# Performance work log

Measured on AMD Instinct MI355X. Metric: run time of the kernel, lower is better.

The kernel has to match this reference:

```python
import jax, jax.numpy as jnp
import numpy as np

WS = 11  # window_size
PAD = WS // 2
C1 = 0.01 ** 2
C2 = 0.03 ** 2
_DN = ('NCHW', 'OIHW', 'NCHW')


def _box_filter(x):
    """Depthwise 11x11 uniform (1/121) box filter with zero padding,
    implemented as two separable 1D depthwise convs (math-identical to
    F.conv2d with the ones/ws^2 window and padding=ws//2)."""
    c = x.shape[1]
    kh = jnp.ones((c, 1, WS, 1), x.dtype) / WS
    kw = jnp.ones((c, 1, 1, WS), x.dtype) / WS
    x = jax.lax.conv_general_dilated(x, kh, (1, 1), [(PAD, PAD), (0, 0)],
                                     feature_group_count=c, dimension_numbers=_DN)
    x = jax.lax.conv_general_dilated(x, kw, (1, 1), [(0, 0), (PAD, PAD)],
                                     feature_group_count=c, dimension_numbers=_DN)
    return x


def setup_inputs() -> dict:
    key = jax.random.key(0)
    k1, k2 = jax.random.split(key)
    shape = (16, 3, 512, 512)
    img1 = jax.random.uniform(k1, shape, dtype=jnp.float32)
    img2 = jax.random.uniform(k2, shape, dtype=jnp.float32)
    return {"img1": img1, "img2": img2}


def reference(img1, img2):
    mu1 = _box_filter(img1)
    mu2 = _box_filter(img2)
    mu1_sq = mu1 * mu1
    mu2_sq = mu2 * mu2
    mu1_mu2 = mu1 * mu2
    sigma1_sq = _box_filter(img1 * img1) - mu1_sq
    sigma2_sq = _box_filter(img2 * img2) - mu2_sq
    sigma12 = _box_filter(img1 * img2) - mu1_mu2
    ssim_map = ((2.0 * mu1_mu2 + C1) * (2.0 * sigma12 + C2)) / (
        (mu1_sq + mu2_sq + C1) * (sigma1_sq + sigma2_sq + C2))
    return 1.0 - jnp.mean(ssim_map)
```

## Files before the change

### kernel.cpp

```cpp
#include <hip/hip_runtime.h>
#include <hip/hip_fp16.h>


#define CAP   28
#define ROWF  132
#define SSTR  (3 * ROWF)
#define C1K   1.4641f
#define C2K   13.1769f

__device__ __forceinline__ int swz(int x) { return x + (x >> 5); }

__launch_bounds__(256, 3)
__global__ void ssim_fused(const float* __restrict__ img1,
                           const float* __restrict__ img2,
                           float* __restrict__ out)
{
    __shared__ unsigned int ring[CAP * SSTR];

    const int x0 = blockIdx.x * 128;
    const int y0 = blockIdx.y * 128;
    const size_t pbase = (size_t)blockIdx.z * (512 * 512);
    const int tid = threadIdx.x;

    const int hj = tid >> 4;
    const int hk = tid & 15;
    const int xl = x0 + hk * 8 - 8;
    const int xs = swz(tid & 127);

    float S0 = 0.f, S1 = 0.f, S2 = 0.f, S3 = 0.f, S4 = 0.f, accs = 0.f;
    int pslot = hj;
    int cbase = 0;

    for (int t = 0; t < 19; ++t) {
        if (tid < 128) {
            if (t < 18) {
                const int rel = 8 * t + hj;
                const int r   = y0 - 5 + rel;
                float a[24], b[24];
                if ((unsigned)r < 512u) {
                    const float* p1 = img1 + pbase + (size_t)r * 512;
                    const float* p2 = img2 + pbase + (size_t)r * 512;
#pragma unroll
                    for (int u = 0; u < 6; ++u) {
                        const int c4 = xl + 4 * u;
                        float4 v1 = {0.f, 0.f, 0.f, 0.f};
                        float4 v2 = {0.f, 0.f, 0.f, 0.f};
                        if ((unsigned)c4 < 512u) {
                            v1 = *(const float4*)(p1 + c4);
                            v2 = *(const float4*)(p2 + c4);
                        }
                        a[4*u] = v1.x; a[4*u+1] = v1.y; a[4*u+2] = v1.z; a[4*u+3] = v1.w;
                        b[4*u] = v2.x; b[4*u+1] = v2.y; b[4*u+2] = v2.z; b[4*u+3] = v2.w;
                    }
                } else {
#pragma unroll
                    for (int u = 0; u < 24; ++u) { a[u] = 0.f; b[u] = 0.f; }
                }

                float w0 = 0.f, w1 = 0.f, w2 = 0.f, w3 = 0.f, w4 = 0.f;
#pragma unroll
                for (int c = 0; c < 11; ++c) {
                    const float av = a[c + 3], bv = b[c + 3];
                    w0 += av; w1 += bv; w2 += av * av; w3 += bv * bv; w4 += av * bv;
                }

                unsigned int* rb = &ring[pslot * SSTR];
#pragma unroll
                for (int i = 0; i < 8; ++i) {
                    const int ad = swz(hk * 8 + i);
                    const __half2 h01 = __floats2half2_rn(w0, w1);
                    const __half2 h23 = __floats2half2_rn(w2, w3);
                    const __half2 h4x = __floats2half2_rn(w4, 0.f);
                    rb[ad]            = *(const unsigned int*)&h01;
                    rb[ad + ROWF]     = *(const unsigned int*)&h23;
                    rb[ad + 2 * ROWF] = *(const unsigned int*)&h4x;
                    if (i < 7) {
                        const float aN = a[14 + i], aO = a[3 + i];
                        const float bN = b[14 + i], bO = b[3 + i];
                        w0 += aN - aO;
                        w1 += bN - bO;
                        w2 += aN * aN - aO * aO;
                        w3 += bN * bN - bO * bO;
                        w4 += aN * bN - aO * bO;
                    }
                }
                pslot += 8; if (pslot >= CAP) pslot -= CAP;
            }
        } else {
            if (t >= 1) {
#pragma unroll
                for (int jj = 0; jj < 8; ++jj) {
                    const int rel = 8 * (t - 1) + jj;
                    int sa = cbase + jj; if (sa >= CAP) sa -= CAP;
                    const unsigned int* ab = &ring[sa * SSTR + xs];
                    const unsigned int u01 = ab[0], u23 = ab[ROWF], u4 = ab[2 * ROWF];
                    const float2 f01 = __half22float2(*(const __half2*)&u01);
                    const float2 f23 = __half22float2(*(const __half2*)&u23);
                    const float2 f4v = __half22float2(*(const __half2*)&u4);
                    S0 += f01.x; S1 += f01.y; S2 += f23.x; S3 += f23.y; S4 += f4v.x;
                    if (rel >= 11) {
                        int ss = sa - 11; if (ss < 0) ss += CAP;
                        const unsigned int* sb = &ring[ss * SSTR + xs];
                        const unsigned int v01 = sb[0], v23 = sb[ROWF], v4 = sb[2 * ROWF];
                        const float2 g01 = __half22float2(*(const __half2*)&v01);
                        const float2 g23 = __half22float2(*(const __half2*)&v23);
                        const float2 g4v = __half22float2(*(const __half2*)&v4);
                        S0 -= g01.x; S1 -= g01.y; S2 -= g23.x; S3 -= g23.y; S4 -= g4v.x;
                    }
                    if (rel >= 10 && rel <= 137) {
                        const float t01 = S0 * S1;
                        const float p0  = S0 * S0, p1 = S1 * S1;
                        const float num = (2.f * t01 + C1K)
                                        * (2.f * (121.f * S4 - t01) + C2K);
                        const float den = (p0 + p1 + C1K)
                                        * (121.f * (S2 + S3) - p0 - p1 + C2K);
                        accs += num * __builtin_amdgcn_rcpf(den);
                    }
                }
                cbase += 8; if (cbase >= CAP) cbase -= CAP;
            }
        }
        __syncthreads();
    }

    float tot = accs;
#pragma unroll
    for (int off = 32; off > 0; off >>= 1)
        tot += __shfl_down(tot, off);
    float* red = (float*)ring;
    if ((tid & 63) == 0) red[tid >> 6] = tot;
    __syncthreads();
    if (tid == 0) {
        const float s = red[0] + red[1] + red[2] + red[3];
        atomicAdd(out, 1.0f / 768.0f - s * (1.0f / 12582912.0f));
    }
}

extern "C" void kernel_launch(void* const* d_in, const int* in_sizes, int n_in,
                              void* d_out, int out_size, void* d_ws, size_t ws_size,
                              hipStream_t stream)
{
    const float* img1 = (const float*)d_in[0];
    const float* img2 = (const float*)d_in[1];
    float* out = (float*)d_out;

    hipMemsetAsync(out, 0, sizeof(float), stream);

    dim3 grid(4, 4, 48);
    ssim_fused<<<grid, dim3(256), 0, stream>>>(img1, img2, out);
}
```

Measured before the change: 144.1 us.

## Shrink tiles to 64x64 and keep vertical sliding-window history in registers

Tiles shrink from 128x128 to 64x64 with 128-thread blocks, which quadruples the grid and shrinks the shared-memory ring buffer. Consumer threads now keep a 16-entry register history of the horizontal sums, so the value leaving the vertical window comes from registers instead of a second LDS read. The aim is more blocks for occupancy and less LDS traffic. In exchange the halo overhead is larger (74 rows loaded per 64 outputs) and register pressure rises.

```diff
diff --git a/kernel.cpp b/kernel.cpp
--- a/kernel.cpp
+++ b/kernel.cpp
@@ -2,126 +2,143 @@
 #include <hip/hip_fp16.h>
 
 
-#define CAP   28
-#define ROWF  132
+#define CAP   17
+#define ROWF  66
 #define SSTR  (3 * ROWF)
 #define C1K   1.4641f
 #define C2K   13.1769f
 
 __device__ __forceinline__ int swz(int x) { return x + (x >> 5); }
 
-__launch_bounds__(256, 3)
+__launch_bounds__(128, 4)
 __global__ void ssim_fused(const float* __restrict__ img1,
                            const float* __restrict__ img2,
                            float* __restrict__ out)
 {
     __shared__ unsigned int ring[CAP * SSTR];
 
-    const int x0 = blockIdx.x * 128;
-    const int y0 = blockIdx.y * 128;
+    const int x0 = blockIdx.x * 64;
+    const int y0 = blockIdx.y * 64;
     const size_t pbase = (size_t)blockIdx.z * (512 * 512);
     const int tid = threadIdx.x;
 
-    const int hj = tid >> 4;
-    const int hk = tid & 15;
+    const int hj = tid >> 3;
+    const int hk = tid & 7;
     const int xl = x0 + hk * 8 - 8;
-    const int xs = swz(tid & 127);
+    const int xs = swz(tid & 63);
 
     float S0 = 0.f, S1 = 0.f, S2 = 0.f, S3 = 0.f, S4 = 0.f, accs = 0.f;
+
+    unsigned int h[16][3];
+#pragma unroll
+    for (int q = 0; q < 16; ++q) { h[q][0] = 0u; h[q][1] = 0u; h[q][2] = 0u; }
+
     int pslot = hj;
     int cbase = 0;
 
-    for (int t = 0; t < 19; ++t) {
-        if (tid < 128) {
-            if (t < 18) {
+#define CONSUME(ODDQ)                                                          \
+    {                                                                          \
+        _Pragma("unroll")                                                      \
+        for (int jj = 0; jj < 8; ++jj) {                                       \
+            const int rel = relbase + jj;                                      \
+            if (rel > 73) break;                                               \
+            int sa = cbase + jj; if (sa >= CAP) sa -= CAP;                     \
+            const unsigned int* ab = &ring[sa * SSTR + xs];                    \
+            const unsigned int u01 = ab[0];                                    \
+            const unsigned int u23 = ab[ROWF];                                 \
+            const unsigned int u4  = ab[2 * ROWF];                             \
+            const float2 f01 = __half22float2(*(const __half2*)&u01);          \
+            const float2 f23 = __half22float2(*(const __half2*)&u23);          \
+            const float2 f4v = __half22float2(*(const __half2*)&u4);           \
+            const int ws = (ODDQ) ? jj : 8 + jj;                               \
+            const int ss = (ODDQ) ? jj + 5 : ((13 + jj) & 15);                 \
+            const unsigned int g01 = h[ss][0], g23 = h[ss][1], g4 = h[ss][2];  \
+            const float2 e01 = __half22float2(*(const __half2*)&g01);          \
+            const float2 e23 = __half22float2(*(const __half2*)&g23);          \
+            const float2 e4v = __half22float2(*(const __half2*)&g4);           \
+            S0 += f01.x - e01.x; S1 += f01.y - e01.y;                          \
+            S2 += f23.x - e23.x; S3 += f23.y - e23.y;                          \
+            S4 += f4v.x - e4v.x;                                               \
+            h[ws][0] = u01; h[ws][1] = u23; h[ws][2] = u4;                     \
+            if (rel >= 10) {                                                   \
+                const float t01 = S0 * S1;                                     \
+                const float p0  = S0 * S0, p1 = S1 * S1;                       \
+                const float num = (2.f * t01 + C1K)                            \
+                                * (2.f * (121.f * S4 - t01) + C2K);            \
+                const float den = (p0 + p1 + C1K)                              \
+                                * (121.f * (S2 + S3) - p0 - p1 + C2K);         \
+                accs += num * __builtin_amdgcn_rcpf(den);                      \
+            }                                                                  \
+        }                                                                      \
+    }
+
+    for (int t = 0; t <= 10; ++t) {
+        if (tid < 64) {
+            if (t <= 9) {
                 const int rel = 8 * t + hj;
-                const int r   = y0 - 5 + rel;
-                float a[24], b[24];
-                if ((unsigned)r < 512u) {
-                    const float* p1 = img1 + pbase + (size_t)r * 512;
-                    const float* p2 = img2 + pbase + (size_t)r * 512;
+                if (rel <= 73) {
+                    const int r = y0 - 5 + rel;
+                    float a[24], b[24];
+                    if ((unsigned)r < 512u) {
+                        const float* p1 = img1 + pbase + (size_t)r * 512;
+                        const float* p2 = img2 + pbase + (size_t)r * 512;
 #pragma unroll
-                    for (int u = 0; u < 6; ++u) {
-                        const int c4 = xl + 4 * u;
-                        float4 v1 = {0.f, 0.f, 0.f, 0.f};
-                        float4 v2 = {0.f, 0.f, 0.f, 0.f};
-                        if ((unsigned)c4 < 512u) {
-                            v1 = *(const float4*)(p1 + c4);
-                            v2 = *(const float4*)(p2 + c4);
+                        for (int u = 0; u < 6; ++u) {
+                            const int c4 = xl + 4 * u;
+                            float4 v1 = {0.f, 0.f, 0.f, 0.f};
+                            float4 v2 = {0.f, 0.f, 0.f, 0.f};
+                            if ((unsigned)c4 < 512u) {
+                                v1 = *(const float4*)(p1 + c4);
+                                v2 = *(const float4*)(p2 + c4);
+                            }
+                            a[4*u] = v1.x; a[4*u+1] = v1.y; a[4*u+2] = v1.z; a[4*u+3] = v1.w;
+                            b[4*u] = v2.x; b[4*u+1] = v2.y; b[4*u+2] = v2.z; b[4*u+3] = v2.w;
                         }
-                        a[4*u] = v1.x; a[4*u+1] = v1.y; a[4*u+2] = v1.z; a[4*u+3] = v1.w;
-                        b[4*u] = v2.x; b[4*u+1] = v2.y; b[4*u+2] = v2.z; b[4*u+3] = v2.w;
+                    } else {
+#pragma unroll
+                        for (int u = 0; u < 24; ++u) { a[u] = 0.f; b[u] = 0.f; }
                     }
-                } else {
+
+                    float w0 = 0.f, w1 = 0.f, w2 = 0.f, w3 = 0.f, w4 = 0.f;
 #pragma unroll
-                    for (int u = 0; u < 24; ++u) { a[u] = 0.f; b[u] = 0.f; }
-                }
+                    for (int c = 0; c < 11; ++c) {
+                        const float av = a[c + 3], bv = b[c + 3];
+                        w0 += av; w1 += bv; w2 += av * av; w3 += bv * bv; w4 += av * bv;
+                    }
 
-                float w0 = 0.f, w1 = 0.f, w2 = 0.f, w3 = 0.f, w4 = 0.f;
+                    unsigned int* rb = &ring[pslot * SSTR];
 #pragma unroll
-                for (int c = 0; c < 11; ++c) {
-                    const float av = a[c + 3], bv = b[c + 3];
-                    w0 += av; w1 += bv; w2 += av * av; w3 += bv * bv; w4 += av * bv;
-                }
-
-                unsigned int* rb = &ring[pslot * SSTR];
-#pragma unroll
-                for (int i = 0; i < 8; ++i) {
-                    const int ad = swz(hk * 8 + i);
-                    const __half2 h01 = __floats2half2_rn(w0, w1);
-                    const __half2 h23 = __floats2half2_rn(w2, w3);
-                    const __half2 h4x = __floats2half2_rn(w4, 0.f);
-                    rb[ad]            = *(const unsigned int*)&h01;
-                    rb[ad + ROWF]     = *(const unsigned int*)&h23;
-                    rb[ad + 2 * ROWF] = *(const unsigned int*)&h4x;
-                    if (i < 7) {
-                        const float aN = a[14 + i], aO = a[3 + i];
-                        const float bN = b[14 + i], bO = b[3 + i];
-                        w0 += aN - aO;
-                        w1 += bN - bO;
-                        w2 += aN * aN - aO * aO;
-                        w3 += bN * bN - bO * bO;
-                        w4 += aN * bN - aO * bO;
+                    for (int i = 0; i < 8; ++i) {
+                        const int ad = swz(hk * 8 + i);
+                        const __half2 h01 = __floats2half2_rn(w0, w1);
+                        const __half2 h23 = __floats2half2_rn(w2, w3);
+                        const __half2 h4x = __floats2half2_rn(w4, 0.f);
+                        rb[ad]            = *(const unsigned int*)&h01;
+                        rb[ad + ROWF]     = *(const unsigned int*)&h23;
+                        rb[ad + 2 * ROWF] = *(const unsigned int*)&h4x;
+                        if (i < 7) {
+                            const float aN = a[14 + i], aO = a[3 + i];
+                            const float bN = b[14 + i], bO = b[3 + i];
+                            w0 += aN - aO;
+                            w1 += bN - bO;
+                            w2 += aN * aN - aO * aO;
+                            w3 += bN * bN - bO * bO;
+                            w4 += aN * bN - aO * bO;
+                        }
                     }
                 }
                 pslot += 8; if (pslot >= CAP) pslot -= CAP;
             }
         } else {
             if (t >= 1) {
-#pragma unroll
-                for (int jj = 0; jj < 8; ++jj) {
-                    const int rel = 8 * (t - 1) + jj;
-                    int sa = cbase + jj; if (sa >= CAP) sa -= CAP;
-                    const unsigned int* ab = &ring[sa * SSTR + xs];
-                    const unsigned int u01 = ab[0], u23 = ab[ROWF], u4 = ab[2 * ROWF];
-                    const float2 f01 = __half22float2(*(const __half2*)&u01);
-                    const float2 f23 = __half22float2(*(const __half2*)&u23);
-                    const float2 f4v = __half22float2(*(const __half2*)&u4);
-                    S0 += f01.x; S1 += f01.y; S2 += f23.x; S3 += f23.y; S4 += f4v.x;
-                    if (rel >= 11) {
-                        int ss = sa - 11; if (ss < 0) ss += CAP;
-                        const unsigned int* sb = &ring[ss * SSTR + xs];
-                        const unsigned int v01 = sb[0], v23 = sb[ROWF], v4 = sb[2 * ROWF];
-                        const float2 g01 = __half22float2(*(const __half2*)&v01);
-                        const float2 g23 = __half22float2(*(const __half2*)&v23);
-                        const float2 g4v = __half22float2(*(const __half2*)&v4);
-                        S0 -= g01.x; S1 -= g01.y; S2 -= g23.x; S3 -= g23.y; S4 -= g4v.x;
-                    }
-                    if (rel >= 10 && rel <= 137) {
-                        const float t01 = S0 * S1;
-                        const float p0  = S0 * S0, p1 = S1 * S1;
-                        const float num = (2.f * t01 + C1K)
-                                        * (2.f * (121.f * S4 - t01) + C2K);
-                        const float den = (p0 + p1 + C1K)
-                                        * (121.f * (S2 + S3) - p0 - p1 + C2K);
-                        accs += num * __builtin_amdgcn_rcpf(den);
-                    }
-                }
+                const int relbase = 8 * (t - 1);
+                if (t & 1) CONSUME(1) else CONSUME(0)
                 cbase += 8; if (cbase >= CAP) cbase -= CAP;
             }
         }
         __syncthreads();
     }
+#undef CONSUME
 
     float tot = accs;
 #pragma unroll
@@ -131,8 +148,8 @@
     if ((tid & 63) == 0) red[tid >> 6] = tot;
     __syncthreads();
     if (tid == 0) {
-        const float s = red[0] + red[1] + red[2] + red[3];
-        atomicAdd(out, 1.0f / 768.0f - s * (1.0f / 12582912.0f));
+        const float s = red[0] + red[1];
+        atomicAdd(out, 1.0f / 3072.0f - s * (1.0f / 12582912.0f));
     }
 }
 
@@ -146,6 +163,6 @@
 
     hipMemsetAsync(out, 0, sizeof(float), stream);
 
-    dim3 grid(4, 4, 48);
-    ssim_fused<<<grid, dim3(256), 0, stream>>>(img1, img2, out);
+    dim3 grid(8, 8, 48);
+    ssim_fused<<<grid, dim3(128), 0, stream>>>(img1, img2, out);
 }
```

After: 192.5 us. +33.5%, slower.

## Shrink tiles to 64x64 with 128-thread blocks and pack ring writes as uint4

Applied to the files above, without the earlier changes.

Tiles shrink from 128x128 to 64x64, so the grid grows to 8x8x48 blocks of 128 threads: one producer wave and one consumer wave. The shared ring drops the swizzle and the wasted half of the third plane. The cross product is now packed two columns per word, and producers store with vectorized uint4 writes. The aim is more blocks for occupancy and load balance, plus fewer LDS store instructions. In exchange, the halo overhead per tile goes up (74 rows loaded for 64 output rows, and wider column halos), the uint4 stores may cause bank conflicts, and the loop has fewer steps to hide latency.

```diff
diff --git a/kernel.cpp b/kernel.cpp
--- a/kernel.cpp
+++ b/kernel.cpp
@@ -2,119 +2,139 @@
 #include <hip/hip_fp16.h>
 
 
-#define CAP   28
-#define ROWF  132
-#define SSTR  (3 * ROWF)
+#define CAP   27
+#define SSTR  164
+#define P1    64
+#define P2    128
 #define C1K   1.4641f
 #define C2K   13.1769f
 
-__device__ __forceinline__ int swz(int x) { return x + (x >> 5); }
+__device__ __forceinline__ unsigned int h2bits(float a, float b) {
+    const __half2 h = __floats2half2_rn(a, b);
+    return *(const unsigned int*)&h;
+}
 
-__launch_bounds__(256, 3)
+__launch_bounds__(128, 3)
 __global__ void ssim_fused(const float* __restrict__ img1,
                            const float* __restrict__ img2,
                            float* __restrict__ out)
 {
     __shared__ unsigned int ring[CAP * SSTR];
 
-    const int x0 = blockIdx.x * 128;
-    const int y0 = blockIdx.y * 128;
+    const int x0 = blockIdx.x * 64;
+    const int y0 = blockIdx.y * 64;
     const size_t pbase = (size_t)blockIdx.z * (512 * 512);
     const int tid = threadIdx.x;
 
-    const int hj = tid >> 4;
-    const int hk = tid & 15;
+    const int hj = (tid & 63) >> 3;
+    const int hk = tid & 7;
     const int xl = x0 + hk * 8 - 8;
-    const int xs = swz(tid & 127);
+    const int col = tid & 63;
 
     float S0 = 0.f, S1 = 0.f, S2 = 0.f, S3 = 0.f, S4 = 0.f, accs = 0.f;
     int pslot = hj;
     int cbase = 0;
 
-    for (int t = 0; t < 19; ++t) {
-        if (tid < 128) {
-            if (t < 18) {
+    for (int t = 0; t <= 10; ++t) {
+        if (tid < 64) {
+            if (t <= 9) {
                 const int rel = 8 * t + hj;
-                const int r   = y0 - 5 + rel;
-                float a[24], b[24];
-                if ((unsigned)r < 512u) {
-                    const float* p1 = img1 + pbase + (size_t)r * 512;
-                    const float* p2 = img2 + pbase + (size_t)r * 512;
+                if (rel <= 73) {
+                    const int r = y0 - 5 + rel;
+                    float a[24], b[24];
+                    if ((unsigned)r < 512u) {
+                        const float* p1 = img1 + pbase + (size_t)r * 512;
+                        const float* p2 = img2 + pbase + (size_t)r * 512;
 #pragma unroll
-                    for (int u = 0; u < 6; ++u) {
-                        const int c4 = xl + 4 * u;
-                        float4 v1 = {0.f, 0.f, 0.f, 0.f};
-                        float4 v2 = {0.f, 0.f, 0.f, 0.f};
-                        if ((unsigned)c4 < 512u) {
-                            v1 = *(const float4*)(p1 + c4);
-                            v2 = *(const float4*)(p2 + c4);
+                        for (int u = 0; u < 6; ++u) {
+                            const int c4 = xl + 4 * u;
+                            float4 v1 = {0.f, 0.f, 0.f, 0.f};
+                            float4 v2 = {0.f, 0.f, 0.f, 0.f};
+                            if ((unsigned)c4 < 512u) {
+                                v1 = *(const float4*)(p1 + c4);
+                                v2 = *(const float4*)(p2 + c4);
+                            }
+                            a[4*u]=v1.x; a[4*u+1]=v1.y; a[4*u+2]=v1.z; a[4*u+3]=v1.w;
+                            b[4*u]=v2.x; b[4*u+1]=v2.y; b[4*u+2]=v2.z; b[4*u+3]=v2.w;
                         }
-                        a[4*u] = v1.x; a[4*u+1] = v1.y; a[4*u+2] = v1.z; a[4*u+3] = v1.w;
-                        b[4*u] = v2.x; b[4*u+1] = v2.y; b[4*u+2] = v2.z; b[4*u+3] = v2.w;
+                    } else {
+#pragma unroll
+                        for (int u = 0; u < 24; ++u) { a[u] = 0.f; b[u] = 0.f; }
                     }
-                } else {
+
+                    float w0=0.f, w1=0.f, w2=0.f, w3=0.f, w4=0.f;
 #pragma unroll
-                    for (int u = 0; u < 24; ++u) { a[u] = 0.f; b[u] = 0.f; }
-                }
+                    for (int c = 0; c < 11; ++c) {
+                        const float av = a[c+3], bv = b[c+3];
+                        w0 += av; w1 += bv; w2 += av*av; w3 += bv*bv; w4 += av*bv;
+                    }
 
-                float w0 = 0.f, w1 = 0.f, w2 = 0.f, w3 = 0.f, w4 = 0.f;
+                    unsigned int u01[8], u23[8], u4p[4];
+                    float w4e = 0.f;
 #pragma unroll
-                for (int c = 0; c < 11; ++c) {
-                    const float av = a[c + 3], bv = b[c + 3];
-                    w0 += av; w1 += bv; w2 += av * av; w3 += bv * bv; w4 += av * bv;
-                }
+                    for (int i = 0; i < 8; ++i) {
+                        u01[i] = h2bits(w0, w1);
+                        u23[i] = h2bits(w2, w3);
+                        if ((i & 1) == 0) w4e = w4;
+                        else u4p[i >> 1] = h2bits(w4e, w4);
+                        if (i < 7) {
+                            const float aN=a[14+i], aO=a[3+i];
+                            const float bN=b[14+i], bO=b[3+i];
+                            w0 += aN - aO;
+                            w1 += bN - bO;
+                            w2 += aN*aN - aO*aO;
+                            w3 += bN*bN - bO*bO;
+                            w4 += aN*bN - aO*bO;
+                        }
+                    }
 
-                unsigned int* rb = &ring[pslot * SSTR];
-#pragma unroll
-                for (int i = 0; i < 8; ++i) {
-                    const int ad = swz(hk * 8 + i);
-                    const __half2 h01 = __floats2half2_rn(w0, w1);
-                    const __half2 h23 = __floats2half2_rn(w2, w3);
-                    const __half2 h4x = __floats2half2_rn(w4, 0.f);
-                    rb[ad]            = *(const unsigned int*)&h01;
-                    rb[ad + ROWF]     = *(const unsigned int*)&h23;
-                    rb[ad + 2 * ROWF] = *(const unsigned int*)&h4x;
-                    if (i < 7) {
-                        const float aN = a[14 + i], aO = a[3 + i];
-                        const float bN = b[14 + i], bO = b[3 + i];
-                        w0 += aN - aO;
-                        w1 += bN - bO;
-                        w2 += aN * aN - aO * aO;
-                        w3 += bN * bN - bO * bO;
-                        w4 += aN * bN - aO * bO;
-                    }
+                    unsigned int* rb = &ring[pslot * SSTR];
+                    *(uint4*)&rb[hk * 8]          = make_uint4(u01[0],u01[1],u01[2],u01[3]);
+                    *(uint4*)&rb[hk * 8 + 4]      = make_uint4(u01[4],u01[5],u01[6],u01[7]);
+                    *(uint4*)&rb[P1 + hk * 8]     = make_uint4(u23[0],u23[1],u23[2],u23[3]);
+                    *(uint4*)&rb[P1 + hk * 8 + 4] = make_uint4(u23[4],u23[5],u23[6],u23[7]);
+                    *(uint4*)&rb[P2 + hk * 4]     = make_uint4(u4p[0],u4p[1],u4p[2],u4p[3]);
                 }
                 pslot += 8; if (pslot >= CAP) pslot -= CAP;
             }
         } else {
             if (t >= 1) {
+                const int relbase = 8 * (t - 1);
 #pragma unroll
                 for (int jj = 0; jj < 8; ++jj) {
-                    const int rel = 8 * (t - 1) + jj;
-                    int sa = cbase + jj; if (sa >= CAP) sa -= CAP;
-                    const unsigned int* ab = &ring[sa * SSTR + xs];
-                    const unsigned int u01 = ab[0], u23 = ab[ROWF], u4 = ab[2 * ROWF];
-                    const float2 f01 = __half22float2(*(const __half2*)&u01);
-                    const float2 f23 = __half22float2(*(const __half2*)&u23);
-                    const float2 f4v = __half22float2(*(const __half2*)&u4);
-                    S0 += f01.x; S1 += f01.y; S2 += f23.x; S3 += f23.y; S4 += f4v.x;
-                    if (rel >= 11) {
-                        int ss = sa - 11; if (ss < 0) ss += CAP;
-                        const unsigned int* sb = &ring[ss * SSTR + xs];
-                        const unsigned int v01 = sb[0], v23 = sb[ROWF], v4 = sb[2 * ROWF];
-                        const float2 g01 = __half22float2(*(const __half2*)&v01);
-                        const float2 g23 = __half22float2(*(const __half2*)&v23);
-                        const float2 g4v = __half22float2(*(const __half2*)&v4);
-                        S0 -= g01.x; S1 -= g01.y; S2 -= g23.x; S3 -= g23.y; S4 -= g4v.x;
-                    }
-                    if (rel >= 10 && rel <= 137) {
-                        const float t01 = S0 * S1;
-                        const float p0  = S0 * S0, p1 = S1 * S1;
-                        const float num = (2.f * t01 + C1K)
-                                        * (2.f * (121.f * S4 - t01) + C2K);
-                        const float den = (p0 + p1 + C1K)
-                                        * (121.f * (S2 + S3) - p0 - p1 + C2K);
-                        accs += num * __builtin_amdgcn_rcpf(den);
+                    const int rel = relbase + jj;
+                    if (rel <= 73) {
+                        int sa = cbase + jj; if (sa >= CAP) sa -= CAP;
+                        const unsigned int* ab = &ring[sa * SSTR];
+                        const unsigned int u01 = ab[col];
+                        const unsigned int u23 = ab[P1 + col];
+                        const unsigned int u4  = ab[P2 + (col >> 1)];
+                        const float2 f01 = __half22float2(*(const __half2*)&u01);
+                        const float2 f23 = __half22float2(*(const __half2*)&u23);
+                        const float2 f4v = __half22float2(*(const __half2*)&u4);
+                        const float q4a = (col & 1) ? f4v.y : f4v.x;
+                        S0 += f01.x; S1 += f01.y; S2 += f23.x; S3 += f23.y; S4 += q4a;
+                        if (rel >= 11) {
+                            int ss = sa - 11; if (ss < 0) ss += CAP;
+                            const unsigned int* sb = &ring[ss * SSTR];
+                            const unsigned int v01 = sb[col];
+                            const unsigned int v23 = sb[P1 + col];
+                            const unsigned int v4  = sb[P2 + (col >> 1)];
+                            const float2 g01 = __half22float2(*(const __half2*)&v01);
+                            const float2 g23 = __half22float2(*(const __half2*)&v23);
+                            const float2 g4v = __half22float2(*(const __half2*)&v4);
+                            const float q4s = (col & 1) ? g4v.y : g4v.x;
+                            S0 -= g01.x; S1 -= g01.y; S2 -= g23.x; S3 -= g23.y; S4 -= q4s;
+                        }
+                        if (rel >= 10) {
+                            const float t01 = S0 * S1;
+                            const float p0 = S0 * S0, p1 = S1 * S1;
+                            const float num = (2.f * t01 + C1K)
+                                            * (2.f * (121.f * S4 - t01) + C2K);
+                            const float den = (p0 + p1 + C1K)
+                                            * (121.f * (S2 + S3) - p0 - p1 + C2K);
+                            accs += num * __builtin_amdgcn_rcpf(den);
+                        }
                     }
                 }
                 cbase += 8; if (cbase >= CAP) cbase -= CAP;
@@ -131,8 +151,8 @@
     if ((tid & 63) == 0) red[tid >> 6] = tot;
     __syncthreads();
     if (tid == 0) {
-        const float s = red[0] + red[1] + red[2] + red[3];
-        atomicAdd(out, 1.0f / 768.0f - s * (1.0f / 12582912.0f));
+        const float s = red[0] + red[1];
+        atomicAdd(out, 1.0f / 3072.0f - s * (1.0f / 12582912.0f));
     }
 }
 
@@ -146,6 +166,6 @@
 
     hipMemsetAsync(out, 0, sizeof(float), stream);
 
-    dim3 grid(4, 4, 48);
-    ssim_fused<<<grid, dim3(256), 0, stream>>>(img1, img2, out);
+    dim3 grid(8, 8, 48);
+    ssim_fused<<<grid, dim3(128), 0, stream>>>(img1, img2, out);
 }
```

New measurement: 176.5 us. +22.4%, slower.
